# Optimization experiments

Hardware: AMD Instinct MI355X
Metric: run time of the kernel (lower is better)

The kernel has to match this reference:

```python
import jax, jax.numpy as jnp
import numpy as np

HIDDEN = 2048
NUM_HEADS = 32
NUM_GROUPS = 8
HEAD_DIM = HIDDEN // NUM_HEADS          # 64
GROUP_DIM = HEAD_DIM * NUM_GROUPS       # 512
HPG = NUM_HEADS // NUM_GROUPS           # heads per group = 4
B, S = 2, 2048


def setup_inputs() -> dict:
    key = jax.random.key(0)
    ks = jax.random.split(key, 6)
    sd = 1.0 / np.sqrt(HIDDEN)
    return {
        "x": jax.random.normal(ks[0], (B, S, HIDDEN), jnp.float32),
        "mask": jnp.ones((1, 1, S, S), jnp.int32),
        "Wq": jax.random.normal(ks[1], (HIDDEN, HIDDEN), jnp.float32) * sd,
        "bq": jnp.zeros((HIDDEN,), jnp.float32),
        "Wk": jax.random.normal(ks[2], (HIDDEN, GROUP_DIM), jnp.float32) * sd,
        "bk": jnp.zeros((GROUP_DIM,), jnp.float32),
        "Wv": jax.random.normal(ks[3], (HIDDEN, GROUP_DIM), jnp.float32) * sd,
        "bv": jnp.zeros((GROUP_DIM,), jnp.float32),
        "Wo": jax.random.normal(ks[4], (HIDDEN, HIDDEN), jnp.float32) * sd,
        "bo": jnp.zeros((HIDDEN,), jnp.float32),
    }


def reference(x, mask, Wq, bq, Wk, bk, Wv, bv, Wo, bo):
    b, s, _ = x.shape
    # projections
    q = x @ Wq + bq                                        # [B,S,H*d]
    k = x @ Wk + bk                                        # [B,S,G*d]
    v = x @ Wv + bv
    # split heads: q heads are group-major (g, p) to match the torch view
    q = q.reshape(b, s, NUM_GROUPS, HPG, HEAD_DIM)         # [B,S,G,P,d]
    k = k.reshape(b, s, NUM_GROUPS, HEAD_DIM)              # [B,S,G,d]
    v = v.reshape(b, s, NUM_GROUPS, HEAD_DIM)
    scale = 1.0 / np.sqrt(HEAD_DIM).astype(np.float32)
    # grouped attention without materializing repeated K/V
    scores = jnp.einsum('bsgpd,btgd->bgpst', q, k) * scale  # [B,G,P,S,T]
    if mask is not None:
        m = mask[:, :, None]                                # [1,1,1,S,T]
        scores = jnp.where(m == 0, jnp.float32(-1e9), scores)
    weights = jax.nn.softmax(scores, axis=-1)
    out = jnp.einsum('bgpst,btgd->bsgpd', weights, v)       # [B,S,G,P,d]
    out = out.reshape(b, s, HIDDEN)
    return out @ Wo + bo
```

## Files before the change

kernel.cpp:

```cpp
#include <hip/hip_runtime.h>
#include <hip/hip_bf16.h>


#define DEVINL __device__ __forceinline__

typedef __attribute__((ext_vector_type(8))) short bf16x8;
typedef __attribute__((ext_vector_type(4))) float f32x4;

DEVINL unsigned short f2bf(float f) {
  unsigned u = __builtin_bit_cast(unsigned, f);
  u += 0x7fffu + ((u >> 16) & 1u);
  return (unsigned short)(u >> 16);
}

DEVINL unsigned pk2bf(float a, float b) {
  __hip_bfloat162 h = __float22bfloat162_rn(float2{a, b});
  unsigned r;
  __builtin_memcpy(&r, &h, 4);
  return r;
}

DEVINL void gl_lds16(const void* g, void* l) {
  __builtin_amdgcn_global_load_lds(
      (const __attribute__((address_space(1))) void*)g,
      (__attribute__((address_space(3))) void*)l, 16, 0, 0);
}

__global__ __launch_bounds__(256)
void prep_k(const float* __restrict__ x,
            const float* __restrict__ Wq, const float* __restrict__ Wk,
            const float* __restrict__ Wv, const float* __restrict__ Wo,
            const int* __restrict__ mask,
            unsigned short* __restrict__ xb,
            unsigned short* __restrict__ WqT, unsigned short* __restrict__ WkT,
            unsigned short* __restrict__ WvT, unsigned short* __restrict__ WoT,
            int* __restrict__ flags)
{
  __shared__ float tile[64][68];
  __shared__ int fl[4];
  int blk = blockIdx.x;
  const int tid = threadIdx.x;
  if (blk < 4096) {
    size_t base = (size_t)blk * 2048 + tid * 8;
    float4 f0 = *(const float4*)&x[base];
    float4 f1 = *(const float4*)&x[base + 4];
    uint4 o;
    o.x = pk2bf(f0.x, f0.y); o.y = pk2bf(f0.z, f0.w);
    o.z = pk2bf(f1.x, f1.y); o.w = pk2bf(f1.z, f1.w);
    *(uint4*)&xb[base] = o;
    return;
  }
  blk -= 4096;
  if (blk >= 2560) {
    int fb = blk - 2560;
    int qt = fb >> 5, tt = fb & 31;
    bool hz = false;
#pragma unroll
    for (int it = 0; it < 8; ++it) {
      int l = it * 1024 + tid * 4;
      int row = l >> 6, col = l & 63;
      int4 mv = *(const int4*)&mask[(size_t)(qt * 128 + row) * 2048 + tt * 64 + col];
      hz |= (mv.x == 0) | (mv.y == 0) | (mv.z == 0) | (mv.w == 0);
    }
    unsigned long long bal = __ballot(hz);
    if ((tid & 63) == 0) fl[tid >> 6] = (bal != 0ull) ? 1 : 0;
    __syncthreads();
    if (tid == 0) flags[fb] = fl[0] | fl[1] | fl[2] | fl[3];
    return;
  }
  const float* W; unsigned short* WT; int N;
  if (blk < 1024)      { W = Wq; WT = WqT; N = 2048; }
  else if (blk < 1280) { W = Wk; WT = WkT; N = 512;  blk -= 1024; }
  else if (blk < 1536) { W = Wv; WT = WvT; N = 512;  blk -= 1280; }
  else                 { W = Wo; WT = WoT; N = 2048; blk -= 1536; }
  const int kt = blk & 31, nt = blk >> 5;
  const int k0 = kt * 64, n0 = nt * 64;
  const int tr = tid >> 4, tc4 = (tid & 15) * 4;
#pragma unroll
  for (int it = 0; it < 4; ++it) {
    int k = it * 16 + tr;
    float4 v = *(const float4*)&W[(size_t)(k0 + k) * N + n0 + tc4];
    tile[tc4 + 0][k] = v.x; tile[tc4 + 1][k] = v.y;
    tile[tc4 + 2][k] = v.z; tile[tc4 + 3][k] = v.w;
  }
  __syncthreads();
#pragma unroll
  for (int it = 0; it < 4; ++it) {
    int n = it * 16 + tr;
    uint2 o;
    o.x = pk2bf(tile[n][tc4 + 0], tile[n][tc4 + 1]);
    o.y = pk2bf(tile[n][tc4 + 2], tile[n][tc4 + 3]);
    *(uint2*)&WT[(size_t)(n0 + n) * 2048 + k0 + tc4] = o;
  }
}

__global__ __launch_bounds__(256)
void mm_qkv(const unsigned short* __restrict__ A,
            const unsigned short* __restrict__ Wt,
            const float* __restrict__ bq, const float* __restrict__ bk,
            const float* __restrict__ bv,
            unsigned short* __restrict__ qb, unsigned short* __restrict__ kb,
            unsigned short* __restrict__ vb)
{
  __shared__ __align__(16) unsigned short As[128 * 32];
  __shared__ __align__(16) unsigned short Bs[128 * 32];
  const int tid = threadIdx.x;
  const int lane = tid & 63, w = tid >> 6;
  const int l15 = lane & 15, quad = lane >> 4;
  const int wm = w & 1, wn = w >> 1;
  const int wg = blockIdx.y * 24 + blockIdx.x;
  const int swz = (wg & 7) * 96 + (wg >> 3);
  const int row0 = (swz / 24) * 128;
  const int col0 = (swz % 24) * 128;

  f32x4 acc[4][4];
#pragma unroll
  for (int mt = 0; mt < 4; ++mt)
#pragma unroll
    for (int nt = 0; nt < 4; ++nt) acc[mt][nt] = (f32x4){0.f, 0.f, 0.f, 0.f};

  const int c0 = tid, c1 = 256 + tid;
  const size_t aoff0 = (size_t)(row0 + (c0 >> 2)) * 2048 + (c0 & 3) * 8;
  const size_t aoff1 = (size_t)(row0 + (c1 >> 2)) * 2048 + (c1 & 3) * 8;
  const size_t boff0 = (size_t)(col0 + (c0 >> 2)) * 2048 + (c0 & 3) * 8;
  const size_t boff1 = (size_t)(col0 + (c1 >> 2)) * 2048 + (c1 & 3) * 8;

  for (int k0 = 0; k0 < 2048; k0 += 32) {
    gl_lds16(A + aoff0 + k0, As + (size_t)c0 * 8);
    gl_lds16(A + aoff1 + k0, As + (size_t)c1 * 8);
    gl_lds16(Wt + boff0 + k0, Bs + (size_t)c0 * 8);
    gl_lds16(Wt + boff1 + k0, Bs + (size_t)c1 * 8);
    __syncthreads();
    bf16x8 af[4], bfr[4];
#pragma unroll
    for (int mt = 0; mt < 4; ++mt)
      af[mt] = *(const bf16x8*)&As[(wm * 64 + mt * 16 + l15) * 32 + quad * 8];
#pragma unroll
    for (int nt = 0; nt < 4; ++nt)
      bfr[nt] = *(const bf16x8*)&Bs[(wn * 64 + nt * 16 + l15) * 32 + quad * 8];
#pragma unroll
    for (int mt = 0; mt < 4; ++mt)
#pragma unroll
      for (int nt = 0; nt < 4; ++nt)
        acc[mt][nt] = __builtin_amdgcn_mfma_f32_16x16x32_bf16(
            af[mt], bfr[nt], acc[mt][nt], 0, 0, 0);
    __syncthreads();
  }

  const int rbase = row0 + wm * 64 + quad * 4;
#pragma unroll
  for (int nt = 0; nt < 4; ++nt) {
    const int cg = col0 + wn * 64 + nt * 16 + l15;
#pragma unroll
    for (int mt = 0; mt < 4; ++mt) {
#pragma unroll
      for (int reg = 0; reg < 4; ++reg) {
        const int r = rbase + mt * 16 + reg;
        const int bb = r >> 11, ss = r & 2047;
        float v = acc[mt][nt][reg];
        if (col0 < 2048) {
          v += bq[cg];
          int g = cg >> 8, p = (cg >> 6) & 3, d = cg & 63;
          qb[(((size_t)((bb * 8 + g) * 4 + p)) * 2048 + ss) * 64 + d] =
              f2bf(v * 0.1803368801111244f);
        } else if (col0 < 2560) {
          int cl = cg - 2048;
          v += bk[cl];
          int g = cl >> 6, d = cl & 63;
          kb[((size_t)(bb * 8 + g) * 2048 + ss) * 64 + d] = f2bf(v);
        } else {
          int cl = cg - 2560;
          v += bv[cl];
          int g = cl >> 6, d = cl & 63;
          vb[((size_t)(bb * 8 + g) * 64 + d) * 2048 + ss] = f2bf(v);
        }
      }
    }
  }
}

__global__ __launch_bounds__(256)
void mm_out(const unsigned short* __restrict__ A,
            const unsigned short* __restrict__ Bt,
            const float* __restrict__ bias, float* __restrict__ Of)
{
  __shared__ __align__(16) unsigned short As[128 * 32];
  __shared__ __align__(16) unsigned short Bs[128 * 32];
  const int tid = threadIdx.x;
  const int lane = tid & 63, w = tid >> 6;
  const int l15 = lane & 15, quad = lane >> 4;
  const int wm = w & 1, wn = w >> 1;
  const int wg = blockIdx.y * 16 + blockIdx.x;
  const int swz = (wg & 7) * 64 + (wg >> 3);
  const int row0 = (swz >> 4) * 128;
  const int col0 = (swz & 15) * 128;

  f32x4 acc[4][4];
#pragma unroll
  for (int mt = 0; mt < 4; ++mt)
#pragma unroll
    for (int nt = 0; nt < 4; ++nt) acc[mt][nt] = (f32x4){0.f, 0.f, 0.f, 0.f};

  const int c0 = tid, c1 = 256 + tid;
  const size_t aoff0 = (size_t)(row0 + (c0 >> 2)) * 2048 + (c0 & 3) * 8;
  const size_t aoff1 = (size_t)(row0 + (c1 >> 2)) * 2048 + (c1 & 3) * 8;
  const size_t boff0 = (size_t)(col0 + (c0 >> 2)) * 2048 + (c0 & 3) * 8;
  const size_t boff1 = (size_t)(col0 + (c1 >> 2)) * 2048 + (c1 & 3) * 8;

  for (int k0 = 0; k0 < 2048; k0 += 32) {
    gl_lds16(A + aoff0 + k0, As + (size_t)c0 * 8);
    gl_lds16(A + aoff1 + k0, As + (size_t)c1 * 8);
    gl_lds16(Bt + boff0 + k0, Bs + (size_t)c0 * 8);
    gl_lds16(Bt + boff1 + k0, Bs + (size_t)c1 * 8);
    __syncthreads();
    bf16x8 af[4], bfr[4];
#pragma unroll
    for (int mt = 0; mt < 4; ++mt)
      af[mt] = *(const bf16x8*)&As[(wm * 64 + mt * 16 + l15) * 32 + quad * 8];
#pragma unroll
    for (int nt = 0; nt < 4; ++nt)
      bfr[nt] = *(const bf16x8*)&Bs[(wn * 64 + nt * 16 + l15) * 32 + quad * 8];
#pragma unroll
    for (int mt = 0; mt < 4; ++mt)
#pragma unroll
      for (int nt = 0; nt < 4; ++nt)
        acc[mt][nt] = __builtin_amdgcn_mfma_f32_16x16x32_bf16(
            af[mt], bfr[nt], acc[mt][nt], 0, 0, 0);
    __syncthreads();
  }

  const int rbase = row0 + wm * 64 + quad * 4;
#pragma unroll
  for (int nt = 0; nt < 4; ++nt) {
    const int cg = col0 + wn * 64 + nt * 16 + l15;
    const float bvv = bias[cg];
#pragma unroll
    for (int mt = 0; mt < 4; ++mt)
#pragma unroll
      for (int reg = 0; reg < 4; ++reg) {
        const int r = rbase + mt * 16 + reg;
        Of[(size_t)r * 2048 + cg] = acc[mt][nt][reg] + bvv;
      }
  }
}

__global__ __launch_bounds__(512, 4)
void attn_k(const unsigned short* __restrict__ qb,
            const unsigned short* __restrict__ kb,
            const unsigned short* __restrict__ vb,
            const int* __restrict__ mask, const int* __restrict__ flags,
            unsigned short* __restrict__ attnb)
{
  __shared__ __align__(16) unsigned short Ks[2][64 * 64];
  __shared__ __align__(16) unsigned short Vs[2][64 * 64];
  __shared__ __align__(16) unsigned short Ps[256 * 72];
  const int tid = threadIdx.x;
  const int lane = tid & 63, w = tid >> 6;
  const int l15 = lane & 15, quad = lane >> 4;

  const int lid = blockIdx.y * 8 + blockIdx.x;
  const int work = (lid & 7) * 64 + (lid >> 3);
  const int qt = work & 7;
  const int pr = work >> 3;
  const int q0 = qt * 256;
  const int b = pr >> 5, g = (pr >> 2) & 7, p = pr & 3;
  const int bg = b * 8 + g;

  const unsigned short* Kg = kb + (size_t)bg * 2048 * 64;
  const unsigned short* Vg = vb + (size_t)bg * 64 * 2048;
  const unsigned short* Qg = qb + (size_t)(bg * 4 + p) * 2048 * 64;

  bf16x8 qf[2][2];
#pragma unroll
  for (int u = 0; u < 2; ++u) {
    const size_t qrow = (size_t)(q0 + w * 32 + u * 16 + l15) * 64;
    qf[u][0] = *(const bf16x8*)&Qg[qrow + quad * 8];
    qf[u][1] = *(const bf16x8*)&Qg[qrow + 32 + quad * 8];
  }

  bf16x8 ones;
#pragma unroll
  for (int i = 0; i < 8; ++i) ones[i] = (short)0x3F80;

  f32x4 acc_o[4][2];
  f32x4 acc_l[2];
#pragma unroll
  for (int u = 0; u < 2; ++u) acc_l[u] = (f32x4){0.f, 0.f, 0.f, 0.f};
#pragma unroll
  for (int dt = 0; dt < 4; ++dt)
#pragma unroll
    for (int u = 0; u < 2; ++u) acc_o[dt][u] = (f32x4){0.f, 0.f, 0.f, 0.f};

  const int kr = tid >> 3;
  const int kx = ((tid & 7) ^ (kr & 7)) * 8;

  gl_lds16(Kg + (size_t)kr * 64 + kx, &Ks[0][(size_t)tid * 8]);
  gl_lds16(Vg + (size_t)kr * 2048 + kx, &Vs[0][(size_t)tid * 8]);
  __syncthreads();

  for (int it = 0; it < 32; ++it) {
    const int cur = it & 1;
    const int t0 = it << 6;
    if (it < 31) {
      const int tn = t0 + 64;
      gl_lds16(Kg + (size_t)(tn + kr) * 64 + kx, &Ks[cur ^ 1][(size_t)tid * 8]);
      gl_lds16(Vg + (size_t)kr * 2048 + tn + kx, &Vs[cur ^ 1][(size_t)tid * 8]);
    }
    const unsigned short* Kc = Ks[cur];
    const unsigned short* Vc = Vs[cur];

    bf16x8 kf[4][2];
#pragma unroll
    for (int nt = 0; nt < 4; ++nt) {
      const int trow = nt * 16 + l15, ks = trow & 7;
      kf[nt][0] = *(const bf16x8*)&Kc[trow * 64 + ((quad ^ ks) * 8)];
      kf[nt][1] = *(const bf16x8*)&Kc[trow * 64 + (((4 + quad) ^ ks) * 8)];
    }
    const bool msk = flags[(qt * 2 + (w >> 2)) * 32 + it] != 0;

#pragma unroll
    for (int u = 0; u < 2; ++u) {
      f32x4 st[4];
      __builtin_amdgcn_s_setprio(1);
#pragma unroll
      for (int nt = 0; nt < 4; ++nt) {
        f32x4 z = (f32x4){0.f, 0.f, 0.f, 0.f};
        z = __builtin_amdgcn_mfma_f32_16x16x32_bf16(kf[nt][0], qf[u][0], z, 0, 0, 0);
        st[nt] = __builtin_amdgcn_mfma_f32_16x16x32_bf16(kf[nt][1], qf[u][1], z, 0, 0, 0);
      }
      __builtin_amdgcn_s_setprio(0);
      if (msk) {
        const size_t mrow = (size_t)(q0 + w * 32 + u * 16 + l15) * 2048;
#pragma unroll
        for (int nt = 0; nt < 4; ++nt) {
          int4 mv = *(const int4*)&mask[mrow + t0 + nt * 16 + quad * 4];
          if (mv.x == 0) st[nt][0] = -1e30f;
          if (mv.y == 0) st[nt][1] = -1e30f;
          if (mv.z == 0) st[nt][2] = -1e30f;
          if (mv.w == 0) st[nt][3] = -1e30f;
        }
      }
      const int srow = w * 32 + u * 16 + l15;
#pragma unroll
      for (int nt = 0; nt < 4; ++nt) {
        float p0 = __builtin_amdgcn_exp2f(st[nt][0]);
        float p1 = __builtin_amdgcn_exp2f(st[nt][1]);
        float p2 = __builtin_amdgcn_exp2f(st[nt][2]);
        float p3 = __builtin_amdgcn_exp2f(st[nt][3]);
        uint2 pkd;
        pkd.x = pk2bf(p0, p1);
        pkd.y = pk2bf(p2, p3);
        *(uint2*)&Ps[srow * 72 + nt * 16 + quad * 4] = pkd;
      }
    }
    asm volatile("s_waitcnt lgkmcnt(0)" ::: "memory");

    bf16x8 pf[2][2];
    __builtin_amdgcn_s_setprio(1);
#pragma unroll
    for (int u = 0; u < 2; ++u) {
      const int srow = w * 32 + u * 16 + l15;
      pf[u][0] = *(const bf16x8*)&Ps[srow * 72 + quad * 8];
      pf[u][1] = *(const bf16x8*)&Ps[srow * 72 + 32 + quad * 8];
      acc_l[u] = __builtin_amdgcn_mfma_f32_16x16x32_bf16(ones, pf[u][0], acc_l[u], 0, 0, 0);
      acc_l[u] = __builtin_amdgcn_mfma_f32_16x16x32_bf16(ones, pf[u][1], acc_l[u], 0, 0, 0);
    }
#pragma unroll
    for (int dt = 0; dt < 4; ++dt) {
      const int drow = dt * 16 + l15, ks = drow & 7;
      bf16x8 v0 = *(const bf16x8*)&Vc[drow * 64 + ((quad ^ ks) * 8)];
      bf16x8 v1 = *(const bf16x8*)&Vc[drow * 64 + (((4 + quad) ^ ks) * 8)];
#pragma unroll
      for (int u = 0; u < 2; ++u) {
        acc_o[dt][u] = __builtin_amdgcn_mfma_f32_16x16x32_bf16(v0, pf[u][0], acc_o[dt][u], 0, 0, 0);
        acc_o[dt][u] = __builtin_amdgcn_mfma_f32_16x16x32_bf16(v1, pf[u][1], acc_o[dt][u], 0, 0, 0);
      }
    }
    __builtin_amdgcn_s_setprio(0);
    __syncthreads();
  }

  const int hh = g * 4 + p;
#pragma unroll
  for (int u = 0; u < 2; ++u) {
    const float inv = 1.0f / acc_l[u][0];
    const int s = q0 + w * 32 + u * 16 + l15;
#pragma unroll
    for (int dt = 0; dt < 4; ++dt) {
      uint2 o;
      o.x = pk2bf(acc_o[dt][u][0] * inv, acc_o[dt][u][1] * inv);
      o.y = pk2bf(acc_o[dt][u][2] * inv, acc_o[dt][u][3] * inv);
      *(uint2*)&attnb[((size_t)(b * 2048 + s)) * 2048 + hh * 64 + dt * 16 + quad * 4] = o;
    }
  }
}

extern "C" void kernel_launch(void* const* d_in, const int* in_sizes, int n_in,
                              void* d_out, int out_size, void* d_ws, size_t ws_size,
                              hipStream_t stream)
{
  (void)in_sizes; (void)n_in; (void)out_size; (void)ws_size;
  const float* x  = (const float*)d_in[0];
  const int* mask = (const int*)d_in[1];
  const float* Wq = (const float*)d_in[2];
  const float* bq = (const float*)d_in[3];
  const float* Wk = (const float*)d_in[4];
  const float* bk = (const float*)d_in[5];
  const float* Wv = (const float*)d_in[6];
  const float* bv = (const float*)d_in[7];
  const float* Wo = (const float*)d_in[8];
  const float* bo = (const float*)d_in[9];
  float* out = (float*)d_out;

  unsigned short* xb  = (unsigned short*)d_ws;
  unsigned short* WqT = xb  + 8388608;
  unsigned short* WkT = WqT + 4194304;
  unsigned short* WvT = WkT + 1048576;
  unsigned short* WoT = WvT + 1048576;
  unsigned short* qb  = WoT + 4194304;
  unsigned short* kb  = qb  + 8388608;
  unsigned short* vb  = kb  + 2097152;
  int* flags = (int*)(vb + 2097152);
  unsigned short* attnb = xb;

  hipLaunchKernelGGL(prep_k, dim3(7168), dim3(256), 0, stream,
                     x, Wq, Wk, Wv, Wo, mask, xb, WqT, WkT, WvT, WoT, flags);
  hipLaunchKernelGGL(mm_qkv, dim3(24, 32), dim3(256), 0, stream,
                     xb, WqT, bq, bk, bv, qb, kb, vb);
  hipLaunchKernelGGL(attn_k, dim3(8, 64), dim3(512), 0, stream,
                     qb, kb, vb, mask, flags, attnb);
  hipLaunchKernelGGL(mm_out, dim3(16, 32), dim3(256), 0, stream,
                     attnb, WoT, bo, out);
}
```

Measured before the change: 335.6 us.

## Double GEMM K-tile to 64 with XOR-swizzled LDS layout; pad transpose tile

Both projection GEMMs now stage 64-wide K slices per iteration instead of 32. That halves the number of barrier pairs and global-to-LDS rounds, and each 16-byte chunk is placed in LDS with an XOR swizzle on the row so fragment reads avoid bank conflicts. The weight-transpose tile padding changes from 68 to 65 floats to reduce bank conflicts in the column-wise writes. LDS per block doubles, which may lower occupancy, and loads are still not double-buffered.

```diff
diff --git a/kernel.cpp b/kernel.cpp
--- a/kernel.cpp
+++ b/kernel.cpp
@@ -36,7 +36,7 @@
             unsigned short* __restrict__ WvT, unsigned short* __restrict__ WoT,
             int* __restrict__ flags)
 {
-  __shared__ float tile[64][68];
+  __shared__ float tile[64][65];
   __shared__ int fl[4];
   int blk = blockIdx.x;
   const int tid = threadIdx.x;
@@ -94,6 +94,42 @@
   }
 }
 
+#define GEMM97_BODY(Aptr, Bptr) \
+  f32x4 acc[4][4]; \
+  _Pragma("unroll") \
+  for (int mt = 0; mt < 4; ++mt) \
+    _Pragma("unroll") \
+    for (int nt = 0; nt < 4; ++nt) acc[mt][nt] = (f32x4){0.f, 0.f, 0.f, 0.f}; \
+  const int srow = tid >> 3; \
+  const int schunk = (tid & 7) ^ (srow & 7); \
+  const unsigned short* Asrc = (Aptr) + (size_t)(row0 + srow) * 2048 + schunk * 8; \
+  const unsigned short* Bsrc = (Bptr) + (size_t)(col0 + srow) * 2048 + schunk * 8; \
+  for (int k0 = 0; k0 < 2048; k0 += 64) { \
+    _Pragma("unroll") \
+    for (int i = 0; i < 4; ++i) { \
+      gl_lds16(Asrc + (size_t)i * 32 * 2048 + k0, As + ((i * 256 + tid) * 8)); \
+      gl_lds16(Bsrc + (size_t)i * 32 * 2048 + k0, Bs + ((i * 256 + tid) * 8)); \
+    } \
+    __syncthreads(); \
+    _Pragma("unroll") \
+    for (int kh = 0; kh < 2; ++kh) { \
+      bf16x8 af[4], bfr[4]; \
+      const int swq = ((kh * 4 + quad) ^ (l15 & 7)) * 8; \
+      _Pragma("unroll") \
+      for (int mt = 0; mt < 4; ++mt) { \
+        af[mt]  = *(const bf16x8*)&As[(wm * 64 + mt * 16 + l15) * 64 + swq]; \
+        bfr[mt] = *(const bf16x8*)&Bs[(wn * 64 + mt * 16 + l15) * 64 + swq]; \
+      } \
+      _Pragma("unroll") \
+      for (int mt = 0; mt < 4; ++mt) \
+        _Pragma("unroll") \
+        for (int nt = 0; nt < 4; ++nt) \
+          acc[mt][nt] = __builtin_amdgcn_mfma_f32_16x16x32_bf16( \
+              af[mt], bfr[nt], acc[mt][nt], 0, 0, 0); \
+    } \
+    __syncthreads(); \
+  }
+
 __global__ __launch_bounds__(256)
 void mm_qkv(const unsigned short* __restrict__ A,
             const unsigned short* __restrict__ Wt,
@@ -102,8 +138,8 @@
             unsigned short* __restrict__ qb, unsigned short* __restrict__ kb,
             unsigned short* __restrict__ vb)
 {
-  __shared__ __align__(16) unsigned short As[128 * 32];
-  __shared__ __align__(16) unsigned short Bs[128 * 32];
+  __shared__ __align__(16) unsigned short As[128 * 64];
+  __shared__ __align__(16) unsigned short Bs[128 * 64];
   const int tid = threadIdx.x;
   const int lane = tid & 63, w = tid >> 6;
   const int l15 = lane & 15, quad = lane >> 4;
@@ -113,39 +149,7 @@
   const int row0 = (swz / 24) * 128;
   const int col0 = (swz % 24) * 128;
 
-  f32x4 acc[4][4];
-#pragma unroll
-  for (int mt = 0; mt < 4; ++mt)
-#pragma unroll
-    for (int nt = 0; nt < 4; ++nt) acc[mt][nt] = (f32x4){0.f, 0.f, 0.f, 0.f};
-
-  const int c0 = tid, c1 = 256 + tid;
-  const size_t aoff0 = (size_t)(row0 + (c0 >> 2)) * 2048 + (c0 & 3) * 8;
-  const size_t aoff1 = (size_t)(row0 + (c1 >> 2)) * 2048 + (c1 & 3) * 8;
-  const size_t boff0 = (size_t)(col0 + (c0 >> 2)) * 2048 + (c0 & 3) * 8;
-  const size_t boff1 = (size_t)(col0 + (c1 >> 2)) * 2048 + (c1 & 3) * 8;
-
-  for (int k0 = 0; k0 < 2048; k0 += 32) {
-    gl_lds16(A + aoff0 + k0, As + (size_t)c0 * 8);
-    gl_lds16(A + aoff1 + k0, As + (size_t)c1 * 8);
-    gl_lds16(Wt + boff0 + k0, Bs + (size_t)c0 * 8);
-    gl_lds16(Wt + boff1 + k0, Bs + (size_t)c1 * 8);
-    __syncthreads();
-    bf16x8 af[4], bfr[4];
-#pragma unroll
-    for (int mt = 0; mt < 4; ++mt)
-      af[mt] = *(const bf16x8*)&As[(wm * 64 + mt * 16 + l15) * 32 + quad * 8];
-#pragma unroll
-    for (int nt = 0; nt < 4; ++nt)
-      bfr[nt] = *(const bf16x8*)&Bs[(wn * 64 + nt * 16 + l15) * 32 + quad * 8];
-#pragma unroll
-    for (int mt = 0; mt < 4; ++mt)
-#pragma unroll
-      for (int nt = 0; nt < 4; ++nt)
-        acc[mt][nt] = __builtin_amdgcn_mfma_f32_16x16x32_bf16(
-            af[mt], bfr[nt], acc[mt][nt], 0, 0, 0);
-    __syncthreads();
-  }
+  GEMM97_BODY(A, Wt)
 
   const int rbase = row0 + wm * 64 + quad * 4;
 #pragma unroll
@@ -184,8 +188,8 @@
             const unsigned short* __restrict__ Bt,
             const float* __restrict__ bias, float* __restrict__ Of)
 {
-  __shared__ __align__(16) unsigned short As[128 * 32];
-  __shared__ __align__(16) unsigned short Bs[128 * 32];
+  __shared__ __align__(16) unsigned short As[128 * 64];
+  __shared__ __align__(16) unsigned short Bs[128 * 64];
   const int tid = threadIdx.x;
   const int lane = tid & 63, w = tid >> 6;
   const int l15 = lane & 15, quad = lane >> 4;
@@ -195,39 +199,7 @@
   const int row0 = (swz >> 4) * 128;
   const int col0 = (swz & 15) * 128;
 
-  f32x4 acc[4][4];
-#pragma unroll
-  for (int mt = 0; mt < 4; ++mt)
-#pragma unroll
-    for (int nt = 0; nt < 4; ++nt) acc[mt][nt] = (f32x4){0.f, 0.f, 0.f, 0.f};
-
-  const int c0 = tid, c1 = 256 + tid;
-  const size_t aoff0 = (size_t)(row0 + (c0 >> 2)) * 2048 + (c0 & 3) * 8;
-  const size_t aoff1 = (size_t)(row0 + (c1 >> 2)) * 2048 + (c1 & 3) * 8;
-  const size_t boff0 = (size_t)(col0 + (c0 >> 2)) * 2048 + (c0 & 3) * 8;
-  const size_t boff1 = (size_t)(col0 + (c1 >> 2)) * 2048 + (c1 & 3) * 8;
-
-  for (int k0 = 0; k0 < 2048; k0 += 32) {
-    gl_lds16(A + aoff0 + k0, As + (size_t)c0 * 8);
-    gl_lds16(A + aoff1 + k0, As + (size_t)c1 * 8);
-    gl_lds16(Bt + boff0 + k0, Bs + (size_t)c0 * 8);
-    gl_lds16(Bt + boff1 + k0, Bs + (size_t)c1 * 8);
-    __syncthreads();
-    bf16x8 af[4], bfr[4];
-#pragma unroll
-    for (int mt = 0; mt < 4; ++mt)
-      af[mt] = *(const bf16x8*)&As[(wm * 64 + mt * 16 + l15) * 32 + quad * 8];
-#pragma unroll
-    for (int nt = 0; nt < 4; ++nt)
-      bfr[nt] = *(const bf16x8*)&Bs[(wn * 64 + nt * 16 + l15) * 32 + quad * 8];
-#pragma unroll
-    for (int mt = 0; mt < 4; ++mt)
-#pragma unroll
-      for (int nt = 0; nt < 4; ++nt)
-        acc[mt][nt] = __builtin_amdgcn_mfma_f32_16x16x32_bf16(
-            af[mt], bfr[nt], acc[mt][nt], 0, 0, 0);
-    __syncthreads();
-  }
+  GEMM97_BODY(A, Bt)
 
   const int rbase = row0 + wm * 64 + quad * 4;
 #pragma unroll
```

After: 348.3 us. 3.8% more time.
